# Kernel optimization log

Hardware: AMD Instinct MI355X
Metric: run time of the kernel (lower is better)

The kernel has to match this reference:

```python
import jax, jax.numpy as jnp
import numpy as np

EPS = 1e-5

def _conv_bn_relu(x, w, gamma, beta):
    # x: [B, C, N], w: [O, C] (1x1 conv, no bias)
    y = jnp.einsum('oc,bcn->bon', w, x)
    # BatchNorm1d in training mode: per-channel stats over (B, N)
    mean = jnp.mean(y, axis=(0, 2), keepdims=True)
    var = jnp.var(y, axis=(0, 2), keepdims=True)
    yhat = (y - mean) * jax.lax.rsqrt(var + EPS)
    return jax.nn.relu(gamma[None, :, None] * yhat + beta[None, :, None])


def setup_inputs() -> dict:
    key = jax.random.key(0)
    ks = jax.random.split(key, 8)
    B, C, N, Cr = 4, 256, 4096, 32
    x = jax.random.normal(ks[0], (B, C, N), dtype=jnp.float32)
    w1 = jax.random.normal(ks[1], (Cr, C), dtype=jnp.float32) * (1.0 / np.sqrt(C))
    w2 = jax.random.normal(ks[2], (Cr, C), dtype=jnp.float32) * (1.0 / np.sqrt(C))
    w3 = jax.random.normal(ks[3], (C, C), dtype=jnp.float32) * (1.0 / np.sqrt(C))
    g1 = 1.0 + 0.1 * jax.random.normal(ks[4], (Cr,), dtype=jnp.float32)
    b1 = 0.1 * jax.random.normal(ks[5], (Cr,), dtype=jnp.float32)
    g2 = 1.0 + 0.1 * jax.random.normal(ks[6], (Cr,), dtype=jnp.float32)
    b2 = 0.1 * jax.random.normal(ks[7], (Cr,), dtype=jnp.float32)
    g3 = jnp.ones((C,), dtype=jnp.float32)
    b3 = jnp.zeros((C,), dtype=jnp.float32)
    return {'x': x, 'w1': w1, 'w2': w2, 'w3': w3,
            'g1': g1, 'b1': b1, 'g2': g2, 'b2': b2, 'g3': g3, 'b3': b3}


def reference(x, w1, w2, w3, g1, b1, g2, b2, g3, b3):
    # a: [B, N, Cr] (queries), k: [B, Cr, N] (keys)
    a = _conv_bn_relu(x, w1, g1, b1).transpose(0, 2, 1)
    k = _conv_bn_relu(x, w2, g2, b2)
    # s[b, n, m] = softmax_m(sum_c a[b,n,c] * k[b,c,m])
    s = jax.nn.softmax(jnp.einsum('bnc,bcm->bnm', a, k), axis=-1)
    d = _conv_bn_relu(x, w3, g3, b3)  # [B, C, N]
    # out = x + d @ s^T : out[b,c,m] = sum_n d[b,c,n] * s[m,n]
    out = x + jnp.einsum('bcn,bmn->bcm', d, s)
    return out
```

## Files before the change

### kernel.cpp

```cpp
#include <hip/hip_runtime.h>
#include <cstddef>
#include <cstdint>

#define B_ 4
#define C_ 256
#define N_ 4096
#define KF_OFF_B  ((size_t)1024 * 1024)
#define DF_OFF_B  ((size_t)2 * 1024 * 1024)
#define SUM_OFF_B ((size_t)10 * 1024 * 1024)
#define ML_OFF_B  (SUM_OFF_B + 1280 * 4)
#define XH_OFF_B  (ML_OFF_B + 524288)
#define XL_OFF_B  (XH_OFF_B + (size_t)8 * 1024 * 1024)
#define WH_OFF_B  (XL_OFF_B + (size_t)8 * 1024 * 1024)
#define WL_OFF_B  (WH_OFF_B + 163840)
#define LOG2E 1.4426950408889634f

typedef unsigned short bfraw;
typedef __attribute__((ext_vector_type(8))) short short8;
typedef __attribute__((ext_vector_type(4))) float float4v;
typedef __attribute__((ext_vector_type(4))) bfraw bfraw4;

__device__ inline bfraw f2bf(float f) {
    union { float f; uint32_t u; } c; c.f = f;
    uint32_t u = c.u;
    u += 0x7fffu + ((u >> 16) & 1u);
    return (bfraw)(u >> 16);
}
__device__ inline float bf2f(bfraw h) {
    union { uint32_t u; float f; } c; c.u = ((uint32_t)h) << 16;
    return c.f;
}
#if __has_builtin(__builtin_amdgcn_exp2f)
__device__ inline float EXP2(float x) { return __builtin_amdgcn_exp2f(x); }
#else
__device__ inline float EXP2(float x) { return exp2f(x); }
#endif
__device__ inline uint32_t pack2(float a, float b) {
    union { float f; uint32_t u; } ca, cb; ca.f = a; cb.f = b;
#if __has_builtin(__builtin_amdgcn_perm)
    return __builtin_amdgcn_perm(cb.u + 0x8000u, ca.u + 0x8000u, 0x07060302u);
#else
    return ((ca.u + 0x8000u) >> 16) | ((cb.u + 0x8000u) & 0xffff0000u);
#endif
}

__global__ void zero_kernel(float* __restrict__ sums) {
    for (int i = threadIdx.x; i < 640; i += 256) sums[i] = 0.f;
}

__global__ __launch_bounds__(256) void wsplit_kernel(
    const float* __restrict__ w1, const float* __restrict__ w2,
    const float* __restrict__ w3, uint8_t* __restrict__ wsb)
{
    bfraw* wh = (bfraw*)(wsb + WH_OFF_B);
    bfraw* wl = (bfraw*)(wsb + WL_OFF_B);
    int idx4 = (blockIdx.x * 256 + threadIdx.x) * 4;
    int ch = idx4 >> 8, k = idx4 & 255;
    const float* wr = (ch < 32) ? (w1 + ch * C_)
                      : (ch < 64) ? (w2 + (ch - 32) * C_)
                                  : (w3 + (ch - 64) * C_);
    float4 v = *(const float4*)&wr[k];
    float va[4] = {v.x, v.y, v.z, v.w};
    bfraw4 h, l;
#pragma unroll
    for (int j = 0; j < 4; ++j) {
        h[j] = f2bf(va[j]);
        l[j] = f2bf(va[j] - bf2f(h[j]));
    }
    *(bfraw4*)&wh[idx4] = h;
    *(bfraw4*)&wl[idx4] = l;
}

__global__ __launch_bounds__(256) void xtsplit_kernel(
    const float* __restrict__ x, uint8_t* __restrict__ wsb)
{
    __shared__ float Ls[64][65];
    bfraw* xh = (bfraw*)(wsb + XH_OFF_B);
    bfraw* xl = (bfraw*)(wsb + XL_OFF_B);
    const int id = blockIdx.x;
    const int b  = id >> 8;
    const int c0 = ((id >> 6) & 3) << 6;
    const int n0 = (id & 63) << 6;
    const int t  = threadIdx.x;
    {
        int cl = t >> 4, nc = (t & 15) << 2;
#pragma unroll
        for (int i = 0; i < 4; ++i) {
            float4 v = *(const float4*)&x[((size_t)b * C_ + c0 + cl + i * 16) * N_ + n0 + nc];
            Ls[cl + i * 16][nc + 0] = v.x;
            Ls[cl + i * 16][nc + 1] = v.y;
            Ls[cl + i * 16][nc + 2] = v.z;
            Ls[cl + i * 16][nc + 3] = v.w;
        }
    }
    __syncthreads();
    int nl = t >> 2, seg = t & 3;
    bfraw hb[16], lb[16];
#pragma unroll
    for (int j = 0; j < 16; ++j) {
        float v = Ls[seg * 16 + j][nl];
        bfraw h = f2bf(v);
        hb[j] = h;
        lb[j] = f2bf(v - bf2f(h));
    }
    size_t base = ((size_t)b * N_ + n0 + nl) * 256 + c0 + seg * 16;
    *(short8*)&xh[base]     = *(short8*)&hb[0];
    *(short8*)&xh[base + 8] = *(short8*)&hb[8];
    *(short8*)&xl[base]     = *(short8*)&lb[0];
    *(short8*)&xl[base + 8] = *(short8*)&lb[8];
}

__global__ __launch_bounds__(256, 2) void ygemm_kernel(uint8_t* __restrict__ wsb)
{
    const bfraw* xh = (const bfraw*)(wsb + XH_OFF_B);
    const bfraw* xl = (const bfraw*)(wsb + XL_OFF_B);
    const bfraw* wh = (const bfraw*)(wsb + WH_OFF_B);
    const bfraw* wl = (const bfraw*)(wsb + WL_OFF_B);
    bfraw* qf  = (bfraw*)wsb;
    bfraw* kfp = (bfraw*)(wsb + KF_OFF_B);
    bfraw* dfp = (bfraw*)(wsb + DF_OFF_B);
    float* sums  = (float*)(wsb + SUM_OFF_B);
    float* sumsq = sums + 320;
    __shared__ float redS[4][64], redQ[4][64];

    const int bx = blockIdx.x;
    const int by = blockIdx.y;
    const int b  = bx >> 5;
    const int n0 = (bx << 7) & (N_ - 1);
    const int t = threadIdx.x, w = t >> 6, l = t & 63, lq = l & 15, lg = l >> 4;
    const int nw = n0 + w * 32;

    float4v acc[4][2];
#pragma unroll
    for (int i = 0; i < 4; ++i)
#pragma unroll
        for (int j = 0; j < 2; ++j) acc[i][j] = (float4v){0.f, 0.f, 0.f, 0.f};

    for (int s = 0; s < 8; ++s) {
        const int k0 = s * 32;
        short8 ah[4], al[4], bh[2], bl[2];
#pragma unroll
        for (int ct = 0; ct < 4; ++ct) {
            size_t off = (size_t)(by * 64 + ct * 16 + lq) * 256 + k0 + lg * 8;
            ah[ct] = *(const short8*)&wh[off];
            al[ct] = *(const short8*)&wl[off];
        }
#pragma unroll
        for (int nt = 0; nt < 2; ++nt) {
            size_t off = ((size_t)b * N_ + nw + nt * 16 + lq) * 256 + k0 + lg * 8;
            bh[nt] = *(const short8*)&xh[off];
            bl[nt] = *(const short8*)&xl[off];
        }
#pragma unroll
        for (int ct = 0; ct < 4; ++ct)
#pragma unroll
            for (int nt = 0; nt < 2; ++nt) {
                acc[ct][nt] = __builtin_amdgcn_mfma_f32_16x16x32_bf16(ah[ct], bh[nt], acc[ct][nt], 0, 0, 0);
                acc[ct][nt] = __builtin_amdgcn_mfma_f32_16x16x32_bf16(al[ct], bh[nt], acc[ct][nt], 0, 0, 0);
                acc[ct][nt] = __builtin_amdgcn_mfma_f32_16x16x32_bf16(ah[ct], bl[nt], acc[ct][nt], 0, 0, 0);
            }
    }
#pragma unroll
    for (int ct = 0; ct < 4; ++ct) {
        float sv[4], qv[4];
#pragma unroll
        for (int r = 0; r < 4; ++r) {
            float a0 = acc[ct][0][r], a1 = acc[ct][1][r];
            sv[r] = a0 + a1;
            qv[r] = a0 * a0 + a1 * a1;
#pragma unroll
            for (int m = 1; m < 16; m <<= 1) {
                sv[r] += __shfl_xor(sv[r], m);
                qv[r] += __shfl_xor(qv[r], m);
            }
        }
        if (lq == 0) {
#pragma unroll
            for (int r = 0; r < 4; ++r) {
                redS[w][ct * 16 + lg * 4 + r] = sv[r];
                redQ[w][ct * 16 + lg * 4 + r] = qv[r];
            }
        }
    }
    __syncthreads();
    if (t < 64) {
        float s = redS[0][t] + redS[1][t] + redS[2][t] + redS[3][t];
        float q = redQ[0][t] + redQ[1][t] + redQ[2][t] + redQ[3][t];
        atomicAdd(&sums[by * 64 + t], s);
        atomicAdd(&sumsq[by * 64 + t], q);
    }
    if (by == 0) {
#pragma unroll
        for (int ct = 0; ct < 4; ++ct)
#pragma unroll
            for (int nt = 0; nt < 2; ++nt)
#pragma unroll
                for (int r = 0; r < 4; ++r) {
                    int c = ct * 16 + lg * 4 + r;
                    int n = nw + nt * 16 + lq;
                    size_t addr = ((size_t)(b << 8) + (n >> 4)) * 512
                                + (size_t)(((n & 15) | (((c >> 3) & 3) << 4)) << 3) + (c & 7);
                    bfraw v = f2bf(acc[ct][nt][r]);
                    if (c < 32) qf[addr] = v; else kfp[addr] = v;
                }
    } else {
#pragma unroll
        for (int ct = 0; ct < 4; ++ct)
#pragma unroll
            for (int nt = 0; nt < 2; ++nt)
#pragma unroll
                for (int r = 0; r < 4; ++r) {
                    int cg = (by - 1) * 64 + ct * 16 + lg * 4 + r;
                    int n = nw + nt * 16 + lq;
                    size_t addr = (((size_t)(b << 4) + (cg >> 4)) * 128 + (n >> 5)) * 512
                                + (size_t)(((cg & 15) | (((n >> 3) & 3) << 4)) << 3) + (n & 7);
                    dfp[addr] = f2bf(acc[ct][nt][r]);
                }
    }
}

__global__ void finalize_kernel(
    const float* __restrict__ g1, const float* __restrict__ b1,
    const float* __restrict__ g2, const float* __restrict__ b2,
    const float* __restrict__ g3, const float* __restrict__ b3,
    float* __restrict__ sums)
{
    int ch = threadIdx.x;
    if (ch >= 320) return;
    const float inv = 1.0f / (float)(B_ * N_);
    float mean = sums[ch] * inv;
    float var = sums[320 + ch] * inv - mean * mean;
    float g, bb;
    if (ch < 32)      { g = g1[ch];      bb = b1[ch]; }
    else if (ch < 64) { g = g2[ch - 32]; bb = b2[ch - 32]; }
    else              { g = g3[ch - 64]; bb = b3[ch - 64]; }
    float sc = g * rsqrtf(var + 1e-5f);
    float bi = bb - sc * mean;
    if (ch < 32) { sc *= LOG2E; bi *= LOG2E; }
    sums[640 + ch] = sc;
    sums[960 + ch] = bi;
}

__global__ __launch_bounds__(256) void affine_kernel(uint8_t* __restrict__ wsb)
{
    bfraw* base = (bfraw*)wsb;
    const float* sc = (const float*)(wsb + SUM_OFF_B) + 640;
    const float* bi = sc + 320;
    size_t i8 = ((size_t)blockIdx.x * 256 + threadIdx.x) * 8;
    bfraw4 v0 = *(bfraw4*)&base[i8];
    bfraw4 v1 = *(bfraw4*)&base[i8 + 4];
    if (i8 < 1048576) {
        int ch0 = (((int)(i8 >> 7)) & 3) * 8 + ((i8 < 524288) ? 0 : 32);
        float4 s0 = *(const float4*)&sc[ch0];
        float4 s1 = *(const float4*)&sc[ch0 + 4];
        float4 c0 = *(const float4*)&bi[ch0];
        float4 c1 = *(const float4*)&bi[ch0 + 4];
        float sa[8] = {s0.x, s0.y, s0.z, s0.w, s1.x, s1.y, s1.z, s1.w};
        float ca[8] = {c0.x, c0.y, c0.z, c0.w, c1.x, c1.y, c1.z, c1.w};
#pragma unroll
        for (int j = 0; j < 4; ++j) {
            v0[j] = f2bf(fmaxf(0.f, fmaf(sa[j],     bf2f(v0[j]), ca[j])));
            v1[j] = f2bf(fmaxf(0.f, fmaf(sa[j + 4], bf2f(v1[j]), ca[j + 4])));
        }
    } else {
        size_t rel = i8 - 1048576;
        int ch = 64 + (((int)(rel >> 16)) & 15) * 16 + (((int)(rel >> 3)) & 15);
        float s = sc[ch], b = bi[ch];
#pragma unroll
        for (int j = 0; j < 4; ++j) {
            v0[j] = f2bf(fmaxf(0.f, fmaf(s, bf2f(v0[j]), b)));
            v1[j] = f2bf(fmaxf(0.f, fmaf(s, bf2f(v1[j]), b)));
        }
    }
    *(bfraw4*)&base[i8] = v0;
    *(bfraw4*)&base[i8 + 4] = v1;
}

__global__ __launch_bounds__(256, 4) void mlpass_kernel(uint8_t* __restrict__ wsb)
{
    const bfraw* qf  = (const bfraw*)wsb;
    const bfraw* kfp = (const bfraw*)(wsb + KF_OFF_B);
    float* mpart = (float*)(wsb + ML_OFF_B);
    float* lpart = mpart + 65536;
    const int id = blockIdx.x;
    const int b = id & 3;
    const int ks = (id >> 2) & 3;
    const int n0q = (id >> 4) << 6;
    const int tid = threadIdx.x;
    const int w = tid >> 6, l = tid & 63, lq = l & 15, lg = l >> 4;
    const short8 qfrag = *(const short8*)&qf[((size_t)(b * 256 + (n0q >> 4) + w)) * 512 + l * 8];

    float mx = -1e30f, sum = 0.f;
    const int tbeg = b * 256 + ks * 64;
    for (int tk = tbeg; tk < tbeg + 64; tk += 8) {
        float4v st[8];
#pragma unroll
        for (int kt = 0; kt < 8; ++kt) {
            short8 kf = *(const short8*)&kfp[((size_t)(tk + kt)) * 512 + l * 8];
            float4v z = {0.f, 0.f, 0.f, 0.f};
            st[kt] = __builtin_amdgcn_mfma_f32_16x16x32_bf16(kf, qfrag, z, 0, 0, 0);
        }
        float m1 = st[0][0];
#pragma unroll
        for (int kt = 0; kt < 8; ++kt)
#pragma unroll
            for (int r = 0; r < 4; ++r) m1 = fmaxf(m1, st[kt][r]);
        float nm = fmaxf(mx, m1);
        float ae = 0.f;
#pragma unroll
        for (int kt = 0; kt < 8; ++kt)
#pragma unroll
            for (int r = 0; r < 4; ++r) ae += EXP2(st[kt][r] - nm);
        sum = sum * EXP2(mx - nm) + ae;
        mx = nm;
    }
#pragma unroll
    for (int m = 16; m < 64; m <<= 1) {
        float mo = __shfl_xor(mx, m);
        float so = __shfl_xor(sum, m);
        float nm = fmaxf(mx, mo);
        sum = sum * EXP2(mx - nm) + so * EXP2(mo - nm);
        mx = nm;
    }
    if (lg == 0) {
        int idx = ks * 16384 + b * N_ + n0q + w * 16 + lq;
        mpart[idx] = mx;
        lpart[idx] = sum;
    }
}

__global__ __launch_bounds__(256, 2) void flash_kernel(
    const float* __restrict__ x, const uint8_t* __restrict__ wsb,
    float* __restrict__ out)
{
    const bfraw* qf  = (const bfraw*)wsb;
    const bfraw* kfp = (const bfraw*)(wsb + KF_OFF_B);
    const bfraw* dfp = (const bfraw*)(wsb + DF_OFF_B);
    const float* mpart = (const float*)(wsb + ML_OFF_B);
    const float* lpart = mpart + 65536;
    __shared__ bfraw Pl[2][64 * 128];

    const int id  = blockIdx.x;
    const int b   = id & 3;
    const int hf  = (id >> 2) & 1;
    const int n0q = (id >> 3) << 6;
    const int tid = threadIdx.x;
    const int w   = tid >> 6;
    const int l   = tid & 63;
    const int lq  = l & 15;
    const int lg  = l >> 4;
    const int sw  = lq & 7;
    const int qp  = w >> 1;
    const int ks_loc = w & 1;
    const int ctg0 = hf * 8 + w;
    const int ctg1 = hf * 8 + 4 + w;

    const short8 qfragA = *(const short8*)&qf[((size_t)(b * 256 + (n0q >> 4) + 2 * qp)) * 512 + l * 8];
    const short8 qfragB = *(const short8*)&qf[((size_t)(b * 256 + (n0q >> 4) + 2 * qp + 1)) * 512 + l * 8];

    float mlqA, mlqB;
#pragma unroll
    for (int qs = 0; qs < 2; ++qs) {
        int qi = b * N_ + n0q + (2 * qp + qs) * 16 + lq;
        float M = -1e30f, ms[4], ls[4];
#pragma unroll
        for (int s = 0; s < 4; ++s) {
            ms[s] = mpart[s * 16384 + qi];
            ls[s] = lpart[s * 16384 + qi];
            M = fmaxf(M, ms[s]);
        }
        float L = 0.f;
#pragma unroll
        for (int s = 0; s < 4; ++s) L += ls[s] * EXP2(ms[s] - M);
        float v = M + __log2f(L);
        if (qs == 0) mlqA = v; else mlqB = v;
    }
    const float4v zA = {-mlqA, -mlqA, -mlqA, -mlqA};
    const float4v zB = {-mlqB, -mlqB, -mlqB, -mlqB};

    float4v acc[2][4];
#pragma unroll
    for (int i = 0; i < 2; ++i)
#pragma unroll
        for (int j = 0; j < 4; ++j) acc[i][j] = (float4v){0.f, 0.f, 0.f, 0.f};

    short8 kfr[4], dfr[2][4];
#pragma unroll
    for (int kt = 0; kt < 4; ++kt)
        kfr[kt] = *(const short8*)&kfp[((size_t)(b * 256 + ks_loc * 4 + kt)) * 512 + l * 8];
#pragma unroll
    for (int ch = 0; ch < 4; ++ch) {
        dfr[0][ch] = *(const short8*)&dfp[(((size_t)(b * 16 + ctg0)) * 128 + ch) * 512 + l * 8];
        dfr[1][ch] = *(const short8*)&dfp[(((size_t)(b * 16 + ctg1)) * 128 + ch) * 512 + l * 8];
    }

    const int qrowA = (2 * qp) * 16 + lq;
    const int qrowB = (2 * qp + 1) * 16 + lq;
    for (int it = 0; it < 32; ++it) {
        const int ib = it & 1;
        const int nit = (it + 1) & 31;
        float4v stA[4], stB[4];
#pragma unroll
        for (int kt = 0; kt < 4; ++kt) {
            stA[kt] = __builtin_amdgcn_mfma_f32_16x16x32_bf16(kfr[kt], qfragA, zA, 0, 0, 0);
            stB[kt] = __builtin_amdgcn_mfma_f32_16x16x32_bf16(kfr[kt], qfragB, zB, 0, 0, 0);
        }
#pragma unroll
        for (int kt = 0; kt < 4; ++kt)
            kfr[kt] = *(const short8*)&kfp[((size_t)(b * 256 + nit * 8 + ks_loc * 4 + kt)) * 512 + l * 8];
#pragma unroll
        for (int kt = 0; kt < 4; ++kt) {
            int g = (2 * (ks_loc * 4 + kt) + (lg >> 1)) ^ sw;
            {
                float e0 = EXP2(stA[kt][0]);
                float e1 = EXP2(stA[kt][1]);
                float e2 = EXP2(stA[kt][2]);
                float e3 = EXP2(stA[kt][3]);
                uint2 pd = {pack2(e0, e1), pack2(e2, e3)};
                *(uint2*)&Pl[ib][qrowA * 128 + g * 8 + (lg & 1) * 4] = pd;
            }
            {
                float e0 = EXP2(stB[kt][0]);
                float e1 = EXP2(stB[kt][1]);
                float e2 = EXP2(stB[kt][2]);
                float e3 = EXP2(stB[kt][3]);
                uint2 pd = {pack2(e0, e1), pack2(e2, e3)};
                *(uint2*)&Pl[ib][qrowB * 128 + g * 8 + (lg & 1) * 4] = pd;
            }
        }
        __syncthreads();
#pragma unroll
        for (int ch = 0; ch < 4; ++ch) {
            short8 bfr[4];
            int g = (ch * 4 + lg) ^ sw;
#pragma unroll
            for (int qt = 0; qt < 4; ++qt)
                bfr[qt] = *(const short8*)&Pl[ib][(qt * 16 + lq) * 128 + g * 8];
            __builtin_amdgcn_s_setprio(1);
#pragma unroll
            for (int qt = 0; qt < 4; ++qt) {
                acc[0][qt] = __builtin_amdgcn_mfma_f32_16x16x32_bf16(dfr[0][ch], bfr[qt], acc[0][qt], 0, 0, 0);
                acc[1][qt] = __builtin_amdgcn_mfma_f32_16x16x32_bf16(dfr[1][ch], bfr[qt], acc[1][qt], 0, 0, 0);
            }
            __builtin_amdgcn_s_setprio(0);
            dfr[0][ch] = *(const short8*)&dfp[(((size_t)(b * 16 + ctg0)) * 128 + nit * 4 + ch) * 512 + l * 8];
            dfr[1][ch] = *(const short8*)&dfp[(((size_t)(b * 16 + ctg1)) * 128 + nit * 4 + ch) * 512 + l * 8];
        }
    }
#pragma unroll
    for (int ct = 0; ct < 2; ++ct) {
        int ctg = ct ? ctg1 : ctg0;
#pragma unroll
        for (int r = 0; r < 4; ++r) {
            int c = ctg * 16 + lg * 4 + r;
            size_t base = ((size_t)b * C_ + c) * N_ + n0q;
#pragma unroll
            for (int qt = 0; qt < 4; ++qt) {
                size_t idx = base + qt * 16 + lq;
                out[idx] = x[idx] + acc[ct][qt][r];
            }
        }
    }
}

extern "C" void kernel_launch(void* const* d_in, const int* in_sizes, int n_in,
                              void* d_out, int out_size, void* d_ws, size_t ws_size,
                              hipStream_t stream) {
    (void)in_sizes; (void)n_in; (void)out_size; (void)ws_size;
    const float* x  = (const float*)d_in[0];
    const float* w1 = (const float*)d_in[1];
    const float* w2 = (const float*)d_in[2];
    const float* w3 = (const float*)d_in[3];
    const float* g1 = (const float*)d_in[4];
    const float* b1 = (const float*)d_in[5];
    const float* g2 = (const float*)d_in[6];
    const float* b2 = (const float*)d_in[7];
    const float* g3 = (const float*)d_in[8];
    const float* b3 = (const float*)d_in[9];
    uint8_t* wsb = (uint8_t*)d_ws;
    float* sums = (float*)(wsb + SUM_OFF_B);
    float* outp = (float*)d_out;

    zero_kernel<<<1, 256, 0, stream>>>(sums);
    wsplit_kernel<<<80, 256, 0, stream>>>(w1, w2, w3, wsb);
    xtsplit_kernel<<<1024, 256, 0, stream>>>(x, wsb);
    ygemm_kernel<<<dim3(128, 5), 256, 0, stream>>>(wsb);
    finalize_kernel<<<1, 320, 0, stream>>>(g1, b1, g2, b2, g3, b3, sums);
    affine_kernel<<<2560, 256, 0, stream>>>(wsb);
    mlpass_kernel<<<1024, 256, 0, stream>>>(wsb);
    flash_kernel<<<512, 256, 0, stream>>>(x, wsb, outp);
}
```

Baseline: 197.4 us.

## Merge channel halves in flash kernel and fold BN finalize/zero kernels

The flash kernel now uses 512-thread blocks that cover all 256 output channels for a 64-query tile. The QK^T scores and exp2 probabilities are computed once per tile instead of once per channel half. The zero-init kernel is merged into wsplit, and the BN finalize kernel is removed by recomputing scale and bias inline in the affine kernel. This cuts launch overhead and redundant softmax work, at the cost of fewer, larger blocks and repeated per-element coefficient math.

```diff
diff --git a/kernel.cpp b/kernel.cpp
--- a/kernel.cpp
+++ b/kernel.cpp
@@ -44,16 +44,16 @@
 #endif
 }
 
-__global__ void zero_kernel(float* __restrict__ sums) {
-    for (int i = threadIdx.x; i < 640; i += 256) sums[i] = 0.f;
-}
-
 __global__ __launch_bounds__(256) void wsplit_kernel(
     const float* __restrict__ w1, const float* __restrict__ w2,
     const float* __restrict__ w3, uint8_t* __restrict__ wsb)
 {
     bfraw* wh = (bfraw*)(wsb + WH_OFF_B);
     bfraw* wl = (bfraw*)(wsb + WL_OFF_B);
+    if (blockIdx.x == 0) {
+        float* sums = (float*)(wsb + SUM_OFF_B);
+        for (int i = threadIdx.x; i < 640; i += 256) sums[i] = 0.f;
+    }
     int idx4 = (blockIdx.x * 256 + threadIdx.x) * 4;
     int ch = idx4 >> 8, k = idx4 & 255;
     const float* wr = (ch < 32) ? (w1 + ch * C_)
@@ -219,44 +219,41 @@
     }
 }
 
-__global__ void finalize_kernel(
-    const float* __restrict__ g1, const float* __restrict__ b1,
-    const float* __restrict__ g2, const float* __restrict__ b2,
-    const float* __restrict__ g3, const float* __restrict__ b3,
-    float* __restrict__ sums)
-{
-    int ch = threadIdx.x;
-    if (ch >= 320) return;
+__device__ inline void bn_coef(const float* __restrict__ sums,
+                               const float* __restrict__ g1, const float* __restrict__ b1,
+                               const float* __restrict__ g2, const float* __restrict__ b2,
+                               const float* __restrict__ g3, const float* __restrict__ b3,
+                               int ch, float& sc, float& bi)
+{
     const float inv = 1.0f / (float)(B_ * N_);
     float mean = sums[ch] * inv;
-    float var = sums[320 + ch] * inv - mean * mean;
+    float var  = sums[320 + ch] * inv - mean * mean;
     float g, bb;
     if (ch < 32)      { g = g1[ch];      bb = b1[ch]; }
     else if (ch < 64) { g = g2[ch - 32]; bb = b2[ch - 32]; }
     else              { g = g3[ch - 64]; bb = b3[ch - 64]; }
-    float sc = g * rsqrtf(var + 1e-5f);
-    float bi = bb - sc * mean;
+    sc = g * rsqrtf(var + 1e-5f);
+    bi = bb - sc * mean;
     if (ch < 32) { sc *= LOG2E; bi *= LOG2E; }
-    sums[640 + ch] = sc;
-    sums[960 + ch] = bi;
-}
-
-__global__ __launch_bounds__(256) void affine_kernel(uint8_t* __restrict__ wsb)
+}
+
+__global__ __launch_bounds__(256) void affine_kernel(
+    uint8_t* __restrict__ wsb,
+    const float* __restrict__ g1, const float* __restrict__ b1,
+    const float* __restrict__ g2, const float* __restrict__ b2,
+    const float* __restrict__ g3, const float* __restrict__ b3)
 {
     bfraw* base = (bfraw*)wsb;
-    const float* sc = (const float*)(wsb + SUM_OFF_B) + 640;
-    const float* bi = sc + 320;
+    const float* sums = (const float*)(wsb + SUM_OFF_B);
     size_t i8 = ((size_t)blockIdx.x * 256 + threadIdx.x) * 8;
     bfraw4 v0 = *(bfraw4*)&base[i8];
     bfraw4 v1 = *(bfraw4*)&base[i8 + 4];
     if (i8 < 1048576) {
         int ch0 = (((int)(i8 >> 7)) & 3) * 8 + ((i8 < 524288) ? 0 : 32);
-        float4 s0 = *(const float4*)&sc[ch0];
-        float4 s1 = *(const float4*)&sc[ch0 + 4];
-        float4 c0 = *(const float4*)&bi[ch0];
-        float4 c1 = *(const float4*)&bi[ch0 + 4];
-        float sa[8] = {s0.x, s0.y, s0.z, s0.w, s1.x, s1.y, s1.z, s1.w};
-        float ca[8] = {c0.x, c0.y, c0.z, c0.w, c1.x, c1.y, c1.z, c1.w};
+        float sa[8], ca[8];
+#pragma unroll
+        for (int j = 0; j < 8; ++j)
+            bn_coef(sums, g1, b1, g2, b2, g3, b3, ch0 + j, sa[j], ca[j]);
 #pragma unroll
         for (int j = 0; j < 4; ++j) {
             v0[j] = f2bf(fmaxf(0.f, fmaf(sa[j],     bf2f(v0[j]), ca[j])));
@@ -265,7 +262,8 @@
     } else {
         size_t rel = i8 - 1048576;
         int ch = 64 + (((int)(rel >> 16)) & 15) * 16 + (((int)(rel >> 3)) & 15);
-        float s = sc[ch], b = bi[ch];
+        float s, b;
+        bn_coef(sums, g1, b1, g2, b2, g3, b3, ch, s, b);
 #pragma unroll
         for (int j = 0; j < 4; ++j) {
             v0[j] = f2bf(fmaxf(0.f, fmaf(s, bf2f(v0[j]), b)));
@@ -329,7 +327,7 @@
     }
 }
 
-__global__ __launch_bounds__(256, 2) void flash_kernel(
+__global__ __launch_bounds__(512) void flash_kernel(
     const float* __restrict__ x, const uint8_t* __restrict__ wsb,
     float* __restrict__ out)
 {
@@ -342,26 +340,23 @@
 
     const int id  = blockIdx.x;
     const int b   = id & 3;
-    const int hf  = (id >> 2) & 1;
-    const int n0q = (id >> 3) << 6;
+    const int n0q = (id >> 2) << 6;
     const int tid = threadIdx.x;
     const int w   = tid >> 6;
     const int l   = tid & 63;
     const int lq  = l & 15;
     const int lg  = l >> 4;
     const int sw  = lq & 7;
-    const int qp  = w >> 1;
-    const int ks_loc = w & 1;
-    const int ctg0 = hf * 8 + w;
-    const int ctg1 = hf * 8 + 4 + w;
-
-    const short8 qfragA = *(const short8*)&qf[((size_t)(b * 256 + (n0q >> 4) + 2 * qp)) * 512 + l * 8];
-    const short8 qfragB = *(const short8*)&qf[((size_t)(b * 256 + (n0q >> 4) + 2 * qp + 1)) * 512 + l * 8];
-
-    float mlqA, mlqB;
-#pragma unroll
-    for (int qs = 0; qs < 2; ++qs) {
-        int qi = b * N_ + n0q + (2 * qp + qs) * 16 + lq;
+    const int qt_s    = w >> 1;
+    const int ks_loc  = w & 1;
+    const int ctg0 = w;
+    const int ctg1 = 8 + w;
+
+    const short8 qfrag = *(const short8*)&qf[((size_t)(b * 256 + (n0q >> 4) + qt_s)) * 512 + l * 8];
+
+    float mlq;
+    {
+        int qi = b * N_ + n0q + qt_s * 16 + lq;
         float M = -1e30f, ms[4], ls[4];
 #pragma unroll
         for (int s = 0; s < 4; ++s) {
@@ -372,11 +367,9 @@
         float L = 0.f;
 #pragma unroll
         for (int s = 0; s < 4; ++s) L += ls[s] * EXP2(ms[s] - M);
-        float v = M + __log2f(L);
-        if (qs == 0) mlqA = v; else mlqB = v;
-    }
-    const float4v zA = {-mlqA, -mlqA, -mlqA, -mlqA};
-    const float4v zB = {-mlqB, -mlqB, -mlqB, -mlqB};
+        mlq = M + __log2f(L);
+    }
+    const float4v zv = {-mlq, -mlq, -mlq, -mlq};
 
     float4v acc[2][4];
 #pragma unroll
@@ -394,39 +387,26 @@
         dfr[1][ch] = *(const short8*)&dfp[(((size_t)(b * 16 + ctg1)) * 128 + ch) * 512 + l * 8];
     }
 
-    const int qrowA = (2 * qp) * 16 + lq;
-    const int qrowB = (2 * qp + 1) * 16 + lq;
+    const int qrow = qt_s * 16 + lq;
     for (int it = 0; it < 32; ++it) {
         const int ib = it & 1;
         const int nit = (it + 1) & 31;
-        float4v stA[4], stB[4];
-#pragma unroll
-        for (int kt = 0; kt < 4; ++kt) {
-            stA[kt] = __builtin_amdgcn_mfma_f32_16x16x32_bf16(kfr[kt], qfragA, zA, 0, 0, 0);
-            stB[kt] = __builtin_amdgcn_mfma_f32_16x16x32_bf16(kfr[kt], qfragB, zB, 0, 0, 0);
-        }
+        float4v st[4];
+#pragma unroll
+        for (int kt = 0; kt < 4; ++kt)
+            st[kt] = __builtin_amdgcn_mfma_f32_16x16x32_bf16(kfr[kt], qfrag, zv, 0, 0, 0);
 #pragma unroll
         for (int kt = 0; kt < 4; ++kt)
             kfr[kt] = *(const short8*)&kfp[((size_t)(b * 256 + nit * 8 + ks_loc * 4 + kt)) * 512 + l * 8];
 #pragma unroll
         for (int kt = 0; kt < 4; ++kt) {
+            float e0 = EXP2(st[kt][0]);
+            float e1 = EXP2(st[kt][1]);
+            float e2 = EXP2(st[kt][2]);
+            float e3 = EXP2(st[kt][3]);
+            uint2 pd = {pack2(e0, e1), pack2(e2, e3)};
             int g = (2 * (ks_loc * 4 + kt) + (lg >> 1)) ^ sw;
-            {
-                float e0 = EXP2(stA[kt][0]);
-                float e1 = EXP2(stA[kt][1]);
-                float e2 = EXP2(stA[kt][2]);
-                float e3 = EXP2(stA[kt][3]);
-                uint2 pd = {pack2(e0, e1), pack2(e2, e3)};
-                *(uint2*)&Pl[ib][qrowA * 128 + g * 8 + (lg & 1) * 4] = pd;
-            }
-            {
-                float e0 = EXP2(stB[kt][0]);
-                float e1 = EXP2(stB[kt][1]);
-                float e2 = EXP2(stB[kt][2]);
-                float e3 = EXP2(stB[kt][3]);
-                uint2 pd = {pack2(e0, e1), pack2(e2, e3)};
-                *(uint2*)&Pl[ib][qrowB * 128 + g * 8 + (lg & 1) * 4] = pd;
-            }
+            *(uint2*)&Pl[ib][qrow * 128 + g * 8 + (lg & 1) * 4] = pd;
         }
         __syncthreads();
 #pragma unroll
@@ -478,15 +458,12 @@
     const float* g3 = (const float*)d_in[8];
     const float* b3 = (const float*)d_in[9];
     uint8_t* wsb = (uint8_t*)d_ws;
-    float* sums = (float*)(wsb + SUM_OFF_B);
     float* outp = (float*)d_out;
 
-    zero_kernel<<<1, 256, 0, stream>>>(sums);
     wsplit_kernel<<<80, 256, 0, stream>>>(w1, w2, w3, wsb);
     xtsplit_kernel<<<1024, 256, 0, stream>>>(x, wsb);
     ygemm_kernel<<<dim3(128, 5), 256, 0, stream>>>(wsb);
-    finalize_kernel<<<1, 320, 0, stream>>>(g1, b1, g2, b2, g3, b3, sums);
-    affine_kernel<<<2560, 256, 0, stream>>>(wsb);
+    affine_kernel<<<2560, 256, 0, stream>>>(wsb, g1, b1, g2, b2, g3, b3);
     mlpass_kernel<<<1024, 256, 0, stream>>>(wsb);
-    flash_kernel<<<512, 256, 0, stream>>>(x, wsb, outp);
-}
+    flash_kernel<<<256, 512, 0, stream>>>(x, wsb, outp);
+}
```

Measured after the change: 184.3 us. -6.6%, faster.
